# Kernel tuning notes

Hardware: AMD Instinct MI355X
Metric: run time of the kernel (lower is better)

The kernel has to match this reference:

```python
import jax, jax.numpy as jnp
import numpy as np

B, T, R = 512, 4096, 16


def setup_inputs() -> dict:
    key = jax.random.key(0)
    k1, k2, k3 = jax.random.split(key, 3)
    pred = jax.random.normal(k1, (B, T, R), dtype=jnp.float32)
    target = jax.random.normal(k2, (B, T, R), dtype=jnp.float32)
    # replicate_mask marks a contiguous prefix of valid replicates (matches
    # the original `pred[b, :, :n_valid]` slicing). Lengths in [0, R].
    lengths = jax.random.randint(k3, (B,), 0, R + 1)
    replicate_mask = (jnp.arange(R)[None, :] < lengths[:, None]).astype(jnp.float32)
    return {"pred": pred, "target": target, "replicate_mask": replicate_mask}


def _masked_var_unbiased(x, m, n_safe):
    # x: [B,T,R], m: [B,1,R], n_safe: [B,1] (clamped >= 2)
    mean = jnp.sum(x * m, axis=-1, keepdims=True) / n_safe[:, :, None]  # [B,T,1]
    sq = jnp.sum(((x - mean) ** 2) * m, axis=-1)  # [B,T]
    return sq / (n_safe - 1.0)  # unbiased (torch var default ddof=1)


def reference(pred, target, replicate_mask):
    weight = 0.1
    n = jnp.sum(replicate_mask, axis=-1)  # [B]
    n_safe = jnp.maximum(n, 2.0)[:, None]  # avoid div-by-zero; masked out below
    m = replicate_mask[:, None, :]  # [B,1,R]
    pred_var = _masked_var_unbiased(pred, m, n_safe)      # [B,T]
    target_var = _masked_var_unbiased(target, m, n_safe)  # [B,T]
    mse = jnp.mean((pred_var - target_var) ** 2, axis=-1)  # [B]
    valid = n > 1.0
    n_multi = jnp.sum(valid.astype(jnp.float32))
    total = jnp.sum(jnp.where(valid, mse, 0.0))
    loss = jnp.where(n_multi > 0, total / jnp.maximum(n_multi, 1.0), 0.0)
    return weight * loss
```

## Files before the change

kernel.cpp:

```cpp
#include <hip/hip_runtime.h>

#define B_DIM 512
#define T_DIM 4096
#define R_DIM 16

__device__ __forceinline__ float hsum4(float4 v) { return (v.x + v.y) + (v.z + v.w); }

__device__ __forceinline__ float masked_dot(float4 x, float4 m) {
    return ((x.x * m.x + x.y * m.y) + (x.z * m.z + x.w * m.w));
}

__device__ __forceinline__ float masked_sq(float4 x, float4 m, float mean) {
    float dx = x.x - mean, dy = x.y - mean, dz = x.z - mean, dw = x.w - mean;
    return ((dx * dx * m.x + dy * dy * m.y) + (dz * dz * m.z + dw * dw * m.w));
}

__global__ __launch_bounds__(B_DIM) void rcl_prep(const float* __restrict__ mask,
                                                  double* __restrict__ acc,
                                                  float* __restrict__ n_multi) {
    __shared__ float red[B_DIM];
    const int b = threadIdx.x;
    const float4* mp = reinterpret_cast<const float4*>(mask) + b * 4;
    float4 m0 = mp[0], m1 = mp[1], m2 = mp[2], m3 = mp[3];
    float n = hsum4(m0) + hsum4(m1) + hsum4(m2) + hsum4(m3);
    red[b] = (n > 1.0f) ? 1.0f : 0.0f;
    __syncthreads();
    for (int s = B_DIM / 2; s > 0; s >>= 1) {
        if (b < s) red[b] += red[b + s];
        __syncthreads();
    }
    if (b == 0) {
        *n_multi = red[0];
        *acc = 0.0;
    }
}

__global__ __launch_bounds__(256) void rcl_main(const float* __restrict__ pred,
                                                const float* __restrict__ targ,
                                                const float* __restrict__ mask,
                                                double* __restrict__ acc) {
    const int row = blockIdx.x * 256 + threadIdx.x;
    const int b = row >> 12;

    const float4* mp = reinterpret_cast<const float4*>(mask) + b * 4;
    float4 m0 = mp[0], m1 = mp[1], m2 = mp[2], m3 = mp[3];
    float n = hsum4(m0) + hsum4(m1) + hsum4(m2) + hsum4(m3);

    float contrib = 0.0f;
    if (n > 1.0f) {
        const float4* pp = reinterpret_cast<const float4*>(pred) + (size_t)row * 4;
        const float4* tp = reinterpret_cast<const float4*>(targ) + (size_t)row * 4;
        float4 p0 = pp[0], p1 = pp[1], p2 = pp[2], p3 = pp[3];
        float4 q0 = tp[0], q1 = tp[1], q2 = tp[2], q3 = tp[3];

        float sp = (masked_dot(p0, m0) + masked_dot(p1, m1)) +
                   (masked_dot(p2, m2) + masked_dot(p3, m3));
        float sq = (masked_dot(q0, m0) + masked_dot(q1, m1)) +
                   (masked_dot(q2, m2) + masked_dot(q3, m3));
        float mean_p = sp / n;
        float mean_q = sq / n;
        float inv_nm1 = 1.0f / (n - 1.0f);
        float vp = ((masked_sq(p0, m0, mean_p) + masked_sq(p1, m1, mean_p)) +
                    (masked_sq(p2, m2, mean_p) + masked_sq(p3, m3, mean_p))) * inv_nm1;
        float vq = ((masked_sq(q0, m0, mean_q) + masked_sq(q1, m1, mean_q)) +
                    (masked_sq(q2, m2, mean_q) + masked_sq(q3, m3, mean_q))) * inv_nm1;
        float d = vp - vq;
        contrib = d * d;
    }

    for (int off = 32; off > 0; off >>= 1)
        contrib += __shfl_down(contrib, off, 64);

    __shared__ float partial[4];
    const int lane = threadIdx.x & 63;
    const int w = threadIdx.x >> 6;
    if (lane == 0) partial[w] = contrib;
    __syncthreads();
    if (threadIdx.x == 0) {
        float s = (partial[0] + partial[1]) + (partial[2] + partial[3]);
        atomicAdd(acc, (double)s);
    }
}

__global__ void rcl_final(const double* __restrict__ acc,
                          const float* __restrict__ n_multi,
                          float* __restrict__ out) {
    double nm = (double)(*n_multi);
    double total = *acc;
    double loss = (nm > 0.0) ? total / ((double)T_DIM * nm) : 0.0;
    out[0] = (float)(0.1 * loss);
}

extern "C" void kernel_launch(void* const* d_in, const int* in_sizes, int n_in,
                              void* d_out, int out_size, void* d_ws, size_t ws_size,
                              hipStream_t stream) {
    const float* pred = (const float*)d_in[0];
    const float* targ = (const float*)d_in[1];
    const float* mask = (const float*)d_in[2];
    float* out = (float*)d_out;

    double* acc = (double*)d_ws;
    float* n_multi = (float*)((char*)d_ws + 8);

    rcl_prep<<<1, B_DIM, 0, stream>>>(mask, acc, n_multi);
    rcl_main<<<(B_DIM * T_DIM) / 256, 256, 0, stream>>>(pred, targ, mask, acc);
    rcl_final<<<1, 1, 0, stream>>>(acc, n_multi, out);
}
```

Before: 298.2 us.

## Split rows across four lanes for coalesced float4 loads and slot-based reduction

The main kernel now assigns each float4 of a row to its own lane, so adjacent threads read adjacent 16-byte chunks instead of each thread reading a 64-byte row. Per-row sums, means and the variance difference are combined with xor shuffles across the four lanes, and each thread handles four rows so several loads are in flight at once. Block partials are spread over 256 double atomic slots instead of one, and the separate prep kernel is replaced by a memset plus a valid-row count in the final kernel. In exchange, rows with fewer than two valid replicates are now loaded in full rather than skipped, and more shuffles are issued per row.

```diff
diff --git a/kernel.cpp b/kernel.cpp
--- a/kernel.cpp
+++ b/kernel.cpp
@@ -2,107 +2,121 @@
 
 #define B_DIM 512
 #define T_DIM 4096
-#define R_DIM 16
+#define NSLOT 256
+#define BLOCKS 8192
+#define THREADS 256
+#define ITER 4
 
 __device__ __forceinline__ float hsum4(float4 v) { return (v.x + v.y) + (v.z + v.w); }
 
-__device__ __forceinline__ float masked_dot(float4 x, float4 m) {
-    return ((x.x * m.x + x.y * m.y) + (x.z * m.z + x.w * m.w));
+__device__ __forceinline__ float mdot(float4 x, float4 m) {
+    return (x.x * m.x + x.y * m.y) + (x.z * m.z + x.w * m.w);
 }
 
-__device__ __forceinline__ float masked_sq(float4 x, float4 m, float mean) {
-    float dx = x.x - mean, dy = x.y - mean, dz = x.z - mean, dw = x.w - mean;
-    return ((dx * dx * m.x + dy * dy * m.y) + (dz * dz * m.z + dw * dw * m.w));
+__device__ __forceinline__ float msq(float4 x, float4 m, float mu) {
+    float a = x.x - mu, b = x.y - mu, c = x.z - mu, d = x.w - mu;
+    return (a * a * m.x + b * b * m.y) + (c * c * m.z + d * d * m.w);
 }
 
-__global__ __launch_bounds__(B_DIM) void rcl_prep(const float* __restrict__ mask,
-                                                  double* __restrict__ acc,
-                                                  float* __restrict__ n_multi) {
-    __shared__ float red[B_DIM];
-    const int b = threadIdx.x;
-    const float4* mp = reinterpret_cast<const float4*>(mask) + b * 4;
-    float4 m0 = mp[0], m1 = mp[1], m2 = mp[2], m3 = mp[3];
-    float n = hsum4(m0) + hsum4(m1) + hsum4(m2) + hsum4(m3);
-    red[b] = (n > 1.0f) ? 1.0f : 0.0f;
+__global__ __launch_bounds__(THREADS) void rcl_main(
+    const float4* __restrict__ pred4, const float4* __restrict__ targ4,
+    const float4* __restrict__ mask4, double* __restrict__ slots)
+{
+    const int tid0 = blockIdx.x * THREADS + threadIdx.x;
+
+    float4 mv[ITER], pv[ITER], qv[ITER];
+#pragma unroll
+    for (int i = 0; i < ITER; i++) {
+        const int g = tid0 + i * (BLOCKS * THREADS);
+        const int row = g >> 2;
+        const int part = g & 3;
+        const int b = row >> 12;
+        mv[i] = mask4[(b << 2) + part];
+        pv[i] = pred4[g];
+        qv[i] = targ4[g];
+    }
+
+    float csum = 0.0f;
+#pragma unroll
+    for (int i = 0; i < ITER; i++) {
+        float n = hsum4(mv[i]);
+        n += __shfl_xor(n, 1, 64);
+        n += __shfl_xor(n, 2, 64);
+
+        float sp = mdot(pv[i], mv[i]);
+        sp += __shfl_xor(sp, 1, 64);
+        sp += __shfl_xor(sp, 2, 64);
+        float sq = mdot(qv[i], mv[i]);
+        sq += __shfl_xor(sq, 1, 64);
+        sq += __shfl_xor(sq, 2, 64);
+
+        float nsafe = fmaxf(n, 2.0f);
+        float mean_p = sp / nsafe;
+        float mean_q = sq / nsafe;
+
+        float vd = msq(pv[i], mv[i], mean_p) - msq(qv[i], mv[i], mean_q);
+        vd += __shfl_xor(vd, 1, 64);
+        vd += __shfl_xor(vd, 2, 64);
+
+        float dd = vd / (nsafe - 1.0f);
+        csum += (n > 1.0f) ? dd * dd * 0.25f : 0.0f;
+    }
+
+    for (int off = 32; off > 0; off >>= 1)
+        csum += __shfl_down(csum, off, 64);
+
+    __shared__ float partial[THREADS / 64];
+    const int lane = threadIdx.x & 63;
+    const int w = threadIdx.x >> 6;
+    if (lane == 0) partial[w] = csum;
     __syncthreads();
-    for (int s = B_DIM / 2; s > 0; s >>= 1) {
-        if (b < s) red[b] += red[b + s];
-        __syncthreads();
-    }
-    if (b == 0) {
-        *n_multi = red[0];
-        *acc = 0.0;
+    if (threadIdx.x == 0) {
+        float s = (partial[0] + partial[1]) + (partial[2] + partial[3]);
+        atomicAdd(&slots[blockIdx.x & (NSLOT - 1)], (double)s);
     }
 }
 
-__global__ __launch_bounds__(256) void rcl_main(const float* __restrict__ pred,
-                                                const float* __restrict__ targ,
-                                                const float* __restrict__ mask,
-                                                double* __restrict__ acc) {
-    const int row = blockIdx.x * 256 + threadIdx.x;
-    const int b = row >> 12;
+__global__ __launch_bounds__(256) void rcl_final(
+    const double* __restrict__ slots, const float4* __restrict__ mask4,
+    float* __restrict__ out)
+{
+    __shared__ double dred[256];
+    __shared__ float fred[256];
+    const int t = threadIdx.x;
 
-    const float4* mp = reinterpret_cast<const float4*>(mask) + b * 4;
-    float4 m0 = mp[0], m1 = mp[1], m2 = mp[2], m3 = mp[3];
-    float n = hsum4(m0) + hsum4(m1) + hsum4(m2) + hsum4(m3);
+    double tot = slots[t];
 
-    float contrib = 0.0f;
-    if (n > 1.0f) {
-        const float4* pp = reinterpret_cast<const float4*>(pred) + (size_t)row * 4;
-        const float4* tp = reinterpret_cast<const float4*>(targ) + (size_t)row * 4;
-        float4 p0 = pp[0], p1 = pp[1], p2 = pp[2], p3 = pp[3];
-        float4 q0 = tp[0], q1 = tp[1], q2 = tp[2], q3 = tp[3];
-
-        float sp = (masked_dot(p0, m0) + masked_dot(p1, m1)) +
-                   (masked_dot(p2, m2) + masked_dot(p3, m3));
-        float sq = (masked_dot(q0, m0) + masked_dot(q1, m1)) +
-                   (masked_dot(q2, m2) + masked_dot(q3, m3));
-        float mean_p = sp / n;
-        float mean_q = sq / n;
-        float inv_nm1 = 1.0f / (n - 1.0f);
-        float vp = ((masked_sq(p0, m0, mean_p) + masked_sq(p1, m1, mean_p)) +
-                    (masked_sq(p2, m2, mean_p) + masked_sq(p3, m3, mean_p))) * inv_nm1;
-        float vq = ((masked_sq(q0, m0, mean_q) + masked_sq(q1, m1, mean_q)) +
-                    (masked_sq(q2, m2, mean_q) + masked_sq(q3, m3, mean_q))) * inv_nm1;
-        float d = vp - vq;
-        contrib = d * d;
+    float cnt = 0.0f;
+    for (int bb = t; bb < B_DIM; bb += 256) {
+        const float4* mp = mask4 + (bb << 2);
+        float nn = (hsum4(mp[0]) + hsum4(mp[1])) + (hsum4(mp[2]) + hsum4(mp[3]));
+        cnt += (nn > 1.0f) ? 1.0f : 0.0f;
     }
 
-    for (int off = 32; off > 0; off >>= 1)
-        contrib += __shfl_down(contrib, off, 64);
-
-    __shared__ float partial[4];
-    const int lane = threadIdx.x & 63;
-    const int w = threadIdx.x >> 6;
-    if (lane == 0) partial[w] = contrib;
+    dred[t] = tot;
+    fred[t] = cnt;
     __syncthreads();
-    if (threadIdx.x == 0) {
-        float s = (partial[0] + partial[1]) + (partial[2] + partial[3]);
-        atomicAdd(acc, (double)s);
+    for (int s = 128; s > 0; s >>= 1) {
+        if (t < s) { dred[t] += dred[t + s]; fred[t] += fred[t + s]; }
+        __syncthreads();
     }
-}
-
-__global__ void rcl_final(const double* __restrict__ acc,
-                          const float* __restrict__ n_multi,
-                          float* __restrict__ out) {
-    double nm = (double)(*n_multi);
-    double total = *acc;
-    double loss = (nm > 0.0) ? total / ((double)T_DIM * nm) : 0.0;
-    out[0] = (float)(0.1 * loss);
+    if (t == 0) {
+        double nm = (double)fred[0];
+        out[0] = (nm > 0.0) ? (float)(0.1 * (dred[0] / ((double)T_DIM * nm))) : 0.0f;
+    }
 }
 
 extern "C" void kernel_launch(void* const* d_in, const int* in_sizes, int n_in,
                               void* d_out, int out_size, void* d_ws, size_t ws_size,
                               hipStream_t stream) {
-    const float* pred = (const float*)d_in[0];
-    const float* targ = (const float*)d_in[1];
-    const float* mask = (const float*)d_in[2];
+    const float4* pred4 = (const float4*)d_in[0];
+    const float4* targ4 = (const float4*)d_in[1];
+    const float4* mask4 = (const float4*)d_in[2];
     float* out = (float*)d_out;
 
-    double* acc = (double*)d_ws;
-    float* n_multi = (float*)((char*)d_ws + 8);
+    double* slots = (double*)d_ws;
 
-    rcl_prep<<<1, B_DIM, 0, stream>>>(mask, acc, n_multi);
-    rcl_main<<<(B_DIM * T_DIM) / 256, 256, 0, stream>>>(pred, targ, mask, acc);
-    rcl_final<<<1, 1, 0, stream>>>(acc, n_multi, out);
+    hipMemsetAsync(d_ws, 0, NSLOT * sizeof(double), stream);
+    rcl_main<<<BLOCKS, THREADS, 0, stream>>>(pred4, targ4, mask4, slots);
+    rcl_final<<<1, 256, 0, stream>>>(slots, mask4, out);
 }
```

Result: faster. 278.3 us (-6.7%).
